# Kernel tuning notes

Hardware: AMD Instinct MI355X
Metric: run time of the kernel (lower is better)

Reference implementation:

```python
import jax, jax.numpy as jnp
import numpy as np

F, K, V, ITERS = 150000, 5, 100000, 5
S = 2 ** K  # factor state space
MLP_SIZE = 2 * ITERS * S + ITERS * 2  # 330
NEG = -1e30
SHIFT = -500.0

# static bit table: bits[state, slot] in {0,1}
_BITS = ((np.arange(S)[:, None] >> np.arange(K)[None, :]) & 1).astype(np.int32)  # [S,K]
_BITS_T = jnp.asarray(_BITS.T)  # [K,S]
# mask bias for grouped logsumexp: bias[slot, b, state] = 0 if bits[state,slot]==b else NEG
_BIAS = jnp.asarray(np.where(_BITS.T[:, None, :] == np.arange(2)[None, :, None], 0.0, NEG).astype(np.float32))  # [K,2,S]


def neg_inf_to_zero(x):
    return jnp.where(jnp.isneginf(x), 0.0, x)


def expand(msg):
    # msg [F,K,2] -> [F,K,S]: broadcast each slot message over factor states by that slot's bit
    return msg[:, jnp.arange(K)[:, None], _BITS_T]


def setup_inputs() -> dict:
    key = jax.random.key(0)
    k0, k1 = jax.random.split(key)
    factor_potentials = jax.random.normal(k0, (F, S), dtype=jnp.float32)
    var_idx = jax.random.randint(k1, (F, K), 0, V, dtype=jnp.int32)
    prv_v2f = jnp.zeros((F, K, 2), jnp.float32)
    prv_f2v = jnp.zeros((F, K, 2), jnp.float32)
    prv_fb = jax.nn.log_softmax(factor_potentials, axis=1)
    # bethe MLP initialized exactly as in the torch module
    lin1_w = jnp.eye(MLP_SIZE, dtype=jnp.float32)
    lin1_b = jnp.zeros((MLP_SIZE,), jnp.float32)
    num_ones = 2 * S + 2
    lin2_w = jnp.zeros((1, MLP_SIZE), jnp.float32).at[0, -num_ones:].set(1.0)
    lin2_b = jnp.zeros((1,), jnp.float32)
    return {"factor_potentials": factor_potentials, "var_idx": var_idx,
            "prv_v2f": prv_v2f, "prv_f2v": prv_f2v, "prv_fb": prv_fb,
            "lin1_w": lin1_w, "lin1_b": lin1_b, "lin2_w": lin2_w, "lin2_b": lin2_b}


def _shifted_relu(x):
    return jnp.maximum(x, SHIFT)


def reference(factor_potentials, var_idx, prv_v2f, prv_f2v, prv_fb, lin1_w, lin1_b, lin2_w, lin2_b):
    var_flat = var_idx.reshape(-1)
    deg = jax.ops.segment_sum(jnp.ones((F * K,), jnp.float32), var_flat, num_segments=V)  # var_degrees
    pooled_states = []
    fb, v2f = prv_fb, prv_v2f
    for _ in range(ITERS):
        # factor->var messages, no double counting: subtract the slot's own incoming message
        scores = fb[:, None, :] - expand(v2f)                    # [F,K,S]
        m = jax.nn.logsumexp(scores[:, :, None, :] + _BIAS[None], axis=-1)  # [F,K,2]
        m = jax.nn.log_softmax(m, axis=-1)
        # var beliefs: gather all incoming factor->var messages
        vb = jax.ops.segment_sum(m.reshape(-1, 2), var_flat, num_segments=V)  # [V,2]
        vb = jax.nn.log_softmax(vb, axis=-1)
        # var->factor messages, no double counting
        v2f = jax.nn.log_softmax(vb[var_idx] - m, axis=-1)        # [F,K,2]
        # factor beliefs
        fb = factor_potentials + expand(v2f).sum(axis=1)          # [F,S]
        fb = fb - jax.nn.logsumexp(fb, axis=1, keepdims=True)
        # pooled Bethe free-energy features for this iteration
        e_fb = jnp.exp(fb)
        energy = jnp.sum(e_fb * neg_inf_to_zero(factor_potentials), axis=0)     # [S]
        fac_ent = -jnp.sum(e_fb * neg_inf_to_zero(fb), axis=0)                  # [S]
        var_term = jnp.sum((deg - 1.0)[:, None] * jnp.exp(vb) * neg_inf_to_zero(vb), axis=0)  # [2]
        pooled_states.append(jnp.concatenate([energy, fac_ent, var_term])[None, :])  # [1, 2S+2]
    x = jnp.concatenate(pooled_states, axis=1)   # [1, MLP_SIZE]
    h = _shifted_relu(x @ lin1_w.T + lin1_b)
    out = _shifted_relu(h @ lin2_w.T + lin2_b)   # [1,1] estimated ln(Z)
    return out
```

## Files before the change

kernel.cpp:

```cpp
#include <hip/hip_runtime.h>

#define F_N   150000
#define K_N   5
#define S_N   32
#define V_N   100000
#define NITER 5
#define MLP_N 330
#define SHIFTV (-500.0f)
#define W_ELL 32

#define FBLK  ((F_N + 255) / 256)
#define GBLK  ((V_N * 8 + 255) / 256)
#define EBLK  ((F_N * K_N + 255) / 256)

__device__ __forceinline__ float lse2(float a, float b) {
    float mx = fmaxf(a, b);
    return mx + __logf(__expf(a - mx) + __expf(b - mx));
}

__global__ __launch_bounds__(256) void k_build(
    const float* __restrict__ prv_fb,
    const float* __restrict__ prv_v2f,
    const int*   __restrict__ vidx,
    float2*      __restrict__ m_out,
    float2*      __restrict__ mell,
    int*         __restrict__ deg,
    int*         __restrict__ ellpos)
{
    int e = blockIdx.x * 256 + threadIdx.x;
    if (e >= F_N * K_N) return;
    int f = e / K_N;
    int k = e - f * K_N;
    int v = vidx[e];

    int pos = atomicAdd(&deg[v], 1);

    float fb[S_N];
    const float4* p4 = reinterpret_cast<const float4*>(prv_fb + (size_t)f * S_N);
    #pragma unroll
    for (int i = 0; i < S_N / 4; ++i) {
        float4 q = p4[i];
        fb[i*4+0] = q.x; fb[i*4+1] = q.y; fb[i*4+2] = q.z; fb[i*4+3] = q.w;
    }
    float M = fb[0];
    #pragma unroll
    for (int s = 1; s < S_N; ++s) M = fmaxf(M, fb[s]);
    float T = 0.0f, S0 = 0.0f;
    #pragma unroll
    for (int s = 0; s < S_N; ++s) {
        float t = __expf(fb[s] - M);
        T += t;
        if (((s >> k) & 1) == 0) S0 += t;
    }
    float v0 = prv_v2f[(size_t)e * 2 + 0];
    float v1 = prv_v2f[(size_t)e * 2 + 1];
    float u0 = __logf(S0)     - v0;
    float u1 = __logf(T - S0) - v1;
    float l  = lse2(u0, u1);
    float2 nm = make_float2(u0 - l, u1 - l);

    m_out[k*F_N + f] = nm;
    int slot = (pos < W_ELL) ? v * W_ELL + pos : V_N * W_ELL;
    ellpos[e] = slot;
    mell[slot] = nm;
}

__global__ __launch_bounds__(256) void k_gather(
    const float2* __restrict__ mell,
    const int*    __restrict__ deg,
    float2*       __restrict__ vb,
    float2*       __restrict__ cpart,
    int iter)
{
    __shared__ float2 wred[4];
    int t = blockIdx.x * 256 + threadIdx.x;
    int v = t >> 3, sub = t & 7;
    int lane = threadIdx.x & 63;

    float a0 = 0.0f, a1 = 0.0f;
    int n = 0;
    if (v < V_N) {
        n = deg[v];
        int nn = n < W_ELL ? n : W_ELL;
        const float2* row = mell + (size_t)v * W_ELL;
        for (int i = sub; i < nn; i += 8) {
            float2 mm = row[i];
            a0 += mm.x; a1 += mm.y;
        }
    }
    a0 += __shfl_xor(a0, 1); a1 += __shfl_xor(a1, 1);
    a0 += __shfl_xor(a0, 2); a1 += __shfl_xor(a1, 2);
    a0 += __shfl_xor(a0, 4); a1 += __shfl_xor(a1, 4);

    float c0 = 0.0f, c1 = 0.0f;
    if (v < V_N && sub == 0) {
        vb[v] = make_float2(a0, a1);
        float l = lse2(a0, a1);
        float b0 = a0 - l, b1 = a1 - l;
        float dm1 = (float)n - 1.0f;
        c0 = dm1 * __expf(b0) * b0;
        c1 = dm1 * __expf(b1) * b1;
    }
    #pragma unroll
    for (int mk = 32; mk >= 1; mk >>= 1) {
        c0 += __shfl_xor(c0, mk);
        c1 += __shfl_xor(c1, mk);
    }
    if (lane == 0) wred[threadIdx.x >> 6] = make_float2(c0, c1);
    __syncthreads();
    if (threadIdx.x == 0) {
        float2 s = wred[0];
        s.x += wred[1].x + wred[2].x + wred[3].x;
        s.y += wred[1].y + wred[2].y + wred[3].y;
        cpart[iter * GBLK + blockIdx.x] = s;
    }
}

template <bool LAST>
__global__ __launch_bounds__(256) void k_iter(
    const float*  __restrict__ pot,
    const int*    __restrict__ vidx,
    const int*    __restrict__ ellpos,
    float2*       __restrict__ m,
    float2*       __restrict__ mell,
    const float2* __restrict__ vb,
    float*        __restrict__ fpart,
    int iter)
{
    const int lane = threadIdx.x & 63;
    __shared__ float red[256];

    int f = blockIdx.x * 256 + threadIdx.x;
    bool valid = f < F_N;
    int fc = valid ? f : (F_N - 1);

    float2 mm[K_N];
    #pragma unroll
    for (int k = 0; k < K_N; ++k) mm[k] = m[k*F_N + fc];
    int vi[K_N];
    #pragma unroll
    for (int k = 0; k < K_N; ++k) vi[k] = vidx[(size_t)fc * K_N + k];

    float v2f[K_N][2];
    #pragma unroll
    for (int k = 0; k < K_N; ++k) {
        float2 b = vb[vi[k]];
        float a0 = b.x - mm[k].x;
        float a1 = b.y - mm[k].y;
        float l = lse2(a0, a1);
        v2f[k][0] = a0 - l;
        v2f[k][1] = a1 - l;
    }

    float fb[S_N];
    const float4* p4 = reinterpret_cast<const float4*>(pot + (size_t)fc * S_N);
    #pragma unroll
    for (int i = 0; i < S_N / 4; ++i) {
        float4 pv = p4[i];
        int s = i * 4;
        fb[s+0] = pv.x + v2f[0][(s+0)&1] + v2f[1][((s+0)>>1)&1] + v2f[2][((s+0)>>2)&1] + v2f[3][((s+0)>>3)&1] + v2f[4][((s+0)>>4)&1];
        fb[s+1] = pv.y + v2f[0][(s+1)&1] + v2f[1][((s+1)>>1)&1] + v2f[2][((s+1)>>2)&1] + v2f[3][((s+1)>>3)&1] + v2f[4][((s+1)>>4)&1];
        fb[s+2] = pv.z + v2f[0][(s+2)&1] + v2f[1][((s+2)>>1)&1] + v2f[2][((s+2)>>2)&1] + v2f[3][((s+2)>>3)&1] + v2f[4][((s+2)>>4)&1];
        fb[s+3] = pv.w + v2f[0][(s+3)&1] + v2f[1][((s+3)>>1)&1] + v2f[2][((s+3)>>2)&1] + v2f[3][((s+3)>>3)&1] + v2f[4][((s+3)>>4)&1];
    }

    float M = fb[0];
    #pragma unroll
    for (int s = 1; s < S_N; ++s) M = fmaxf(M, fb[s]);

    float T = 0.0f;
    float S0[K_N] = {0.f, 0.f, 0.f, 0.f, 0.f};
    #pragma unroll
    for (int s = 0; s < S_N; ++s) {
        float t = __expf(fb[s] - M);
        T += t;
        #pragma unroll
        for (int k = 0; k < K_N; ++k)
            if (((s >> k) & 1) == 0) S0[k] += t;
    }

    if (!LAST) {
        int el[K_N];
        #pragma unroll
        for (int k = 0; k < K_N; ++k) el[k] = ellpos[(size_t)fc * K_N + k];
        #pragma unroll
        for (int k = 0; k < K_N; ++k) {
            float u0 = __logf(S0[k])     - v2f[k][0];
            float u1 = __logf(T - S0[k]) - v2f[k][1];
            float l  = lse2(u0, u1);
            if (valid) {
                float2 nm = make_float2(u0 - l, u1 - l);
                m[k*F_N + f] = nm;
                mell[el[k]]  = nm;
            }
        }
    }

    float invT = 1.0f / T;
    float logT = __logf(T);
    float arr[2 * S_N];
    #pragma unroll
    for (int s = 0; s < S_N; ++s) {
        float p   = __expf(fb[s] - M) * invT;
        float fbn = fb[s] - M - logT;
        float w   = v2f[0][s&1] + v2f[1][(s>>1)&1] + v2f[2][(s>>2)&1]
                  + v2f[3][(s>>3)&1] + v2f[4][(s>>4)&1];
        float po  = fb[s] - w;
        arr[s]       = valid ? p * po   : 0.0f;
        arr[S_N + s] = valid ? -p * fbn : 0.0f;
    }

    #pragma unroll
    for (int mk = 32; mk >= 1; mk >>= 1) {
        bool upper = (lane & mk) != 0;
        #pragma unroll
        for (int j = 0; j < mk; ++j) {
            float send = upper ? arr[j] : arr[j + mk];
            float recv = __shfl_xor(send, mk);
            float keep = upper ? arr[j + mk] : arr[j];
            arr[j] = keep + recv;
        }
    }

    red[threadIdx.x] = arr[0];
    __syncthreads();
    if (threadIdx.x < 64) {
        float s = red[threadIdx.x] + red[64 + threadIdx.x]
                + red[128 + threadIdx.x] + red[192 + threadIdx.x];
        fpart[((size_t)iter * FBLK + blockIdx.x) * 64 + threadIdx.x] = s;
    }
}

__global__ __launch_bounds__(256) void k_vt(
    const float*  __restrict__ fpart,
    const float2* __restrict__ cpart,
    float*        __restrict__ x)
{
    __shared__ float red[256];
    int b = blockIdx.x, t = threadIdx.x;
    float acc = 0.0f;
    if (b < 320) {
        int it = b >> 6, s = b & 63;
        for (int i = t; i < FBLK; i += 256)
            acc += fpart[((size_t)it * FBLK + i) * 64 + s];
    } else {
        int idx = b - 320;
        int it = idx >> 1, c = idx & 1;
        for (int i = t; i < GBLK; i += 256) {
            float2 p = cpart[it * GBLK + i];
            acc += c ? p.y : p.x;
        }
    }
    red[t] = acc;
    __syncthreads();
    #pragma unroll
    for (int off = 128; off >= 1; off >>= 1) {
        if (t < off) red[t] += red[t + off];
        __syncthreads();
    }
    if (t == 0) {
        if (b < 320) {
            int it = b >> 6, s = b & 63;
            x[it*66 + s] = red[0];
        } else {
            int idx = b - 320;
            int it = idx >> 1, c = idx & 1;
            x[it*66 + 64 + c] = red[0];
        }
    }
}

__global__ __launch_bounds__(64) void k_mlp1(
    const float* __restrict__ x, const float* __restrict__ w1,
    const float* __restrict__ b1, float* __restrict__ h)
{
    int j = blockIdx.x;
    int lane = threadIdx.x;
    float s = 0.0f;
    for (int i = lane; i < MLP_N; i += 64) s += x[i] * w1[(size_t)j * MLP_N + i];
    #pragma unroll
    for (int mk = 32; mk >= 1; mk >>= 1) s += __shfl_xor(s, mk);
    if (lane == 0) h[j] = fmaxf(s + b1[j], SHIFTV);
}

__global__ __launch_bounds__(64) void k_mlp2(
    const float* __restrict__ h, const float* __restrict__ w2,
    const float* __restrict__ b2, float* __restrict__ out)
{
    int lane = threadIdx.x;
    float s = 0.0f;
    for (int i = lane; i < MLP_N; i += 64) s += h[i] * w2[i];
    #pragma unroll
    for (int mk = 32; mk >= 1; mk >>= 1) s += __shfl_xor(s, mk);
    if (lane == 0) out[0] = fmaxf(s + b2[0], SHIFTV);
}

extern "C" void kernel_launch(void* const* d_in, const int* in_sizes, int n_in,
                              void* d_out, int out_size, void* d_ws, size_t ws_size,
                              hipStream_t stream)
{
    (void)in_sizes; (void)n_in; (void)out_size; (void)ws_size;
    const float* pot  = (const float*)d_in[0];
    const int*   vidx = (const int*)  d_in[1];
    const float* pv2f = (const float*)d_in[2];
    const float* pfb  = (const float*)d_in[4];
    const float* w1   = (const float*)d_in[5];
    const float* b1   = (const float*)d_in[6];
    const float* w2   = (const float*)d_in[7];
    const float* b2   = (const float*)d_in[8];

    float2* m      = (float2*)d_ws;
    float2* mell   = m + 5 * F_N;
    float2* vb     = mell + (size_t)V_N * W_ELL + 32;
    float2* cpart  = vb + V_N;
    float*  fpart  = (float*)(cpart + NITER * GBLK);
    float*  x      = fpart + (size_t)NITER * FBLK * 64;
    float*  h      = x + MLP_N;
    int*    ellpos = (int*)(h + MLP_N);
    int*    deg    = ellpos + (size_t)F_N * K_N;

    hipMemsetAsync(deg, 0, (size_t)V_N * sizeof(int), stream);

    k_build<<<EBLK, 256, 0, stream>>>(pfb, pv2f, vidx, m, mell, deg, ellpos);

    for (int it = 0; it < NITER; ++it) {
        k_gather<<<GBLK, 256, 0, stream>>>(mell, deg, vb, cpart, it);
        if (it < NITER - 1)
            k_iter<false><<<FBLK, 256, 0, stream>>>(pot, vidx, ellpos, m, mell, vb, fpart, it);
        else
            k_iter<true><<<FBLK, 256, 0, stream>>>(pot, vidx, ellpos, m, mell, vb, fpart, it);
    }

    k_vt<<<330, 256, 0, stream>>>(fpart, cpart, x);
    k_mlp1<<<MLP_N, 64, 0, stream>>>(x, w1, b1, h);
    k_mlp2<<<1, 64, 0, stream>>>(h, w2, b2, (float*)d_out);
}
```

Baseline: 199.6 us.

## Gather messages via index list instead of duplicated ELL copy; split reduction in halves

Instead of scattering each factor-to-variable message into a second ELL-layout buffer, the build kernel records the message's index in a per-variable entry list. The gather kernel then reads messages indirectly from the single message array. This removes the scattered duplicate write and the ellpos read in every iteration, at the cost of an extra indirection and random reads during the gather. The per-block reduction of the 64 pooled features is also split into two 32-wide passes to cut the live register array, which adds extra barriers.

```diff
diff --git a/kernel.cpp b/kernel.cpp
--- a/kernel.cpp
+++ b/kernel.cpp
@@ -22,10 +22,9 @@
     const float* __restrict__ prv_fb,
     const float* __restrict__ prv_v2f,
     const int*   __restrict__ vidx,
-    float2*      __restrict__ m_out,
-    float2*      __restrict__ mell,
+    float2*      __restrict__ m2,
     int*         __restrict__ deg,
-    int*         __restrict__ ellpos)
+    int*         __restrict__ entries)
 {
     int e = blockIdx.x * 256 + threadIdx.x;
     if (e >= F_N * K_N) return;
@@ -57,17 +56,16 @@
     float u0 = __logf(S0)     - v0;
     float u1 = __logf(T - S0) - v1;
     float l  = lse2(u0, u1);
-    float2 nm = make_float2(u0 - l, u1 - l);
-
-    m_out[k*F_N + f] = nm;
+    m2[k*F_N + f] = make_float2(u0 - l, u1 - l);
+
     int slot = (pos < W_ELL) ? v * W_ELL + pos : V_N * W_ELL;
-    ellpos[e] = slot;
-    mell[slot] = nm;
+    entries[slot] = k * F_N + f;
 }
 
 __global__ __launch_bounds__(256) void k_gather(
-    const float2* __restrict__ mell,
+    const float2* __restrict__ m2,
     const int*    __restrict__ deg,
+    const int*    __restrict__ entries,
     float2*       __restrict__ vb,
     float2*       __restrict__ cpart,
     int iter)
@@ -82,9 +80,9 @@
     if (v < V_N) {
         n = deg[v];
         int nn = n < W_ELL ? n : W_ELL;
-        const float2* row = mell + (size_t)v * W_ELL;
+        const int* row = entries + (size_t)v * W_ELL;
         for (int i = sub; i < nn; i += 8) {
-            float2 mm = row[i];
+            float2 mm = m2[row[i]];
             a0 += mm.x; a1 += mm.y;
         }
     }
@@ -120,9 +118,7 @@
 __global__ __launch_bounds__(256) void k_iter(
     const float*  __restrict__ pot,
     const int*    __restrict__ vidx,
-    const int*    __restrict__ ellpos,
-    float2*       __restrict__ m,
-    float2*       __restrict__ mell,
+    float2*       __restrict__ m2,
     const float2* __restrict__ vb,
     float*        __restrict__ fpart,
     int iter)
@@ -136,7 +132,7 @@
 
     float2 mm[K_N];
     #pragma unroll
-    for (int k = 0; k < K_N; ++k) mm[k] = m[k*F_N + fc];
+    for (int k = 0; k < K_N; ++k) mm[k] = m2[k*F_N + fc];
     int vi[K_N];
     #pragma unroll
     for (int k = 0; k < K_N; ++k) vi[k] = vidx[(size_t)fc * K_N + k];
@@ -180,55 +176,94 @@
     }
 
     if (!LAST) {
-        int el[K_N];
-        #pragma unroll
-        for (int k = 0; k < K_N; ++k) el[k] = ellpos[(size_t)fc * K_N + k];
         #pragma unroll
         for (int k = 0; k < K_N; ++k) {
             float u0 = __logf(S0[k])     - v2f[k][0];
             float u1 = __logf(T - S0[k]) - v2f[k][1];
             float l  = lse2(u0, u1);
-            if (valid) {
-                float2 nm = make_float2(u0 - l, u1 - l);
-                m[k*F_N + f] = nm;
-                mell[el[k]]  = nm;
-            }
+            if (valid) m2[k*F_N + f] = make_float2(u0 - l, u1 - l);
         }
     }
 
     float invT = 1.0f / T;
     float logT = __logf(T);
-    float arr[2 * S_N];
-    #pragma unroll
-    for (int s = 0; s < S_N; ++s) {
-        float p   = __expf(fb[s] - M) * invT;
-        float fbn = fb[s] - M - logT;
-        float w   = v2f[0][s&1] + v2f[1][(s>>1)&1] + v2f[2][(s>>2)&1]
-                  + v2f[3][(s>>3)&1] + v2f[4][(s>>4)&1];
-        float po  = fb[s] - w;
-        arr[s]       = valid ? p * po   : 0.0f;
-        arr[S_N + s] = valid ? -p * fbn : 0.0f;
-    }
-
-    #pragma unroll
-    for (int mk = 32; mk >= 1; mk >>= 1) {
-        bool upper = (lane & mk) != 0;
-        #pragma unroll
-        for (int j = 0; j < mk; ++j) {
-            float send = upper ? arr[j] : arr[j + mk];
-            float recv = __shfl_xor(send, mk);
-            float keep = upper ? arr[j + mk] : arr[j];
-            arr[j] = keep + recv;
-        }
-    }
-
-    red[threadIdx.x] = arr[0];
-    __syncthreads();
-    if (threadIdx.x < 64) {
-        float s = red[threadIdx.x] + red[64 + threadIdx.x]
-                + red[128 + threadIdx.x] + red[192 + threadIdx.x];
-        fpart[((size_t)iter * FBLK + blockIdx.x) * 64 + threadIdx.x] = s;
-    }
+    size_t fbase = ((size_t)iter * FBLK + blockIdx.x) * 64;
+
+    {
+        float arr[S_N];
+        #pragma unroll
+        for (int s = 0; s < S_N; ++s) {
+            float p = __expf(fb[s] - M) * invT;
+            float w = v2f[0][s&1] + v2f[1][(s>>1)&1] + v2f[2][(s>>2)&1]
+                    + v2f[3][(s>>3)&1] + v2f[4][(s>>4)&1];
+            arr[s] = valid ? p * (fb[s] - w) : 0.0f;
+        }
+        {
+            bool upper = (lane & 32) != 0;
+            #pragma unroll
+            for (int j = 0; j < 32; ++j) {
+                float send = upper ? arr[j] : 0.0f;
+                float recv = __shfl_xor(send, 32);
+                arr[j] = (upper ? 0.0f : arr[j]) + recv;
+            }
+        }
+        #pragma unroll
+        for (int mk = 16; mk >= 1; mk >>= 1) {
+            bool upper = (lane & mk) != 0;
+            #pragma unroll
+            for (int j = 0; j < 16; ++j) {
+                if (j < mk) {
+                    float send = upper ? arr[j] : arr[j + mk];
+                    float recv = __shfl_xor(send, mk);
+                    float keep = upper ? arr[j + mk] : arr[j];
+                    arr[j] = keep + recv;
+                }
+            }
+        }
+        red[threadIdx.x] = arr[0];
+    }
+    __syncthreads();
+    if (threadIdx.x < 32)
+        fpart[fbase + threadIdx.x] = red[threadIdx.x] + red[64 + threadIdx.x]
+                                   + red[128 + threadIdx.x] + red[192 + threadIdx.x];
+    __syncthreads();
+
+    {
+        float arr[S_N];
+        #pragma unroll
+        for (int s = 0; s < S_N; ++s) {
+            float p   = __expf(fb[s] - M) * invT;
+            float fbn = fb[s] - M - logT;
+            arr[s] = valid ? -p * fbn : 0.0f;
+        }
+        {
+            bool upper = (lane & 32) != 0;
+            #pragma unroll
+            for (int j = 0; j < 32; ++j) {
+                float send = upper ? arr[j] : 0.0f;
+                float recv = __shfl_xor(send, 32);
+                arr[j] = (upper ? 0.0f : arr[j]) + recv;
+            }
+        }
+        #pragma unroll
+        for (int mk = 16; mk >= 1; mk >>= 1) {
+            bool upper = (lane & mk) != 0;
+            #pragma unroll
+            for (int j = 0; j < 16; ++j) {
+                if (j < mk) {
+                    float send = upper ? arr[j] : arr[j + mk];
+                    float recv = __shfl_xor(send, mk);
+                    float keep = upper ? arr[j + mk] : arr[j];
+                    arr[j] = keep + recv;
+                }
+            }
+        }
+        red[threadIdx.x] = arr[0];
+    }
+    __syncthreads();
+    if (threadIdx.x < 32)
+        fpart[fbase + 32 + threadIdx.x] = red[threadIdx.x] + red[64 + threadIdx.x]
+                                        + red[128 + threadIdx.x] + red[192 + threadIdx.x];
 }
 
 __global__ __launch_bounds__(256) void k_vt(
@@ -309,26 +344,25 @@
     const float* w2   = (const float*)d_in[7];
     const float* b2   = (const float*)d_in[8];
 
-    float2* m      = (float2*)d_ws;
-    float2* mell   = m + 5 * F_N;
-    float2* vb     = mell + (size_t)V_N * W_ELL + 32;
-    float2* cpart  = vb + V_N;
-    float*  fpart  = (float*)(cpart + NITER * GBLK);
-    float*  x      = fpart + (size_t)NITER * FBLK * 64;
-    float*  h      = x + MLP_N;
-    int*    ellpos = (int*)(h + MLP_N);
-    int*    deg    = ellpos + (size_t)F_N * K_N;
+    float2* m2      = (float2*)d_ws;
+    float2* vb      = m2 + 5 * F_N;
+    float2* cpart   = vb + V_N;
+    float*  fpart   = (float*)(cpart + NITER * GBLK);
+    float*  x       = fpart + (size_t)NITER * FBLK * 64;
+    float*  h       = x + MLP_N;
+    int*    entries = (int*)(h + MLP_N);
+    int*    deg     = entries + (size_t)V_N * W_ELL + 64;
 
     hipMemsetAsync(deg, 0, (size_t)V_N * sizeof(int), stream);
 
-    k_build<<<EBLK, 256, 0, stream>>>(pfb, pv2f, vidx, m, mell, deg, ellpos);
+    k_build<<<EBLK, 256, 0, stream>>>(pfb, pv2f, vidx, m2, deg, entries);
 
     for (int it = 0; it < NITER; ++it) {
-        k_gather<<<GBLK, 256, 0, stream>>>(mell, deg, vb, cpart, it);
+        k_gather<<<GBLK, 256, 0, stream>>>(m2, deg, entries, vb, cpart, it);
         if (it < NITER - 1)
-            k_iter<false><<<FBLK, 256, 0, stream>>>(pot, vidx, ellpos, m, mell, vb, fpart, it);
+            k_iter<false><<<FBLK, 256, 0, stream>>>(pot, vidx, m2, vb, fpart, it);
         else
-            k_iter<true><<<FBLK, 256, 0, stream>>>(pot, vidx, ellpos, m, mell, vb, fpart, it);
+            k_iter<true><<<FBLK, 256, 0, stream>>>(pot, vidx, m2, vb, fpart, it);
     }
 
     k_vt<<<330, 256, 0, stream>>>(fpart, cpart, x);
```

After: 404.0 us. +102.4%, slower.
